# Kernel optimization log

Measured on AMD Instinct MI355X. Metric: run time of the kernel, lower is better.

The kernel has to match this reference:

```python
import jax, jax.numpy as jnp
import numpy as np

NUM_ORI = 8      # num_orientations
P = 7            # pooled height/width (out_size)
S = 2            # num_samples (sampling grid per bin side)
SCALE = 0.25     # spatial_scale
CLOCKWISE = False


def setup_inputs() -> dict:
    key = jax.random.key(0)
    kf, kb, kc, ks, ka = jax.random.split(key, 5)
    B, C, H, W = 2, 256, 256, 256   # C = 32 channel groups x 8 orientations
    R = 512
    features = jax.random.normal(kf, (B, C, H, W), dtype=jnp.float32)
    img = H / SCALE                 # image-space extent (1024)
    batch_idx = jax.random.randint(kb, (R,), 0, B).astype(jnp.float32)
    ctr = jax.random.uniform(kc, (R, 2), minval=0.0, maxval=img)
    wh = jax.random.uniform(ks, (R, 2), minval=32.0, maxval=img * 0.25)
    ang = jax.random.uniform(ka, (R,), minval=-np.pi, maxval=np.pi)
    rois = jnp.concatenate([batch_idx[:, None], ctr, wh, ang[:, None]], axis=1)
    return {"features": features, "rois": rois}


def _riroi_align_rotated(features, rois):
    B, C, H, W = features.shape
    O = NUM_ORI
    Cg = C // O
    R = rois.shape[0]
    f32 = features.dtype

    b = rois[:, 0].astype(jnp.int32)
    cx = rois[:, 1] * SCALE
    cy = rois[:, 2] * SCALE
    rw = jnp.maximum(rois[:, 3] * SCALE, 1.0)
    rh = jnp.maximum(rois[:, 4] * SCALE, 1.0)
    theta = rois[:, 5]

    # --- orientation channel alignment (uses original-sign theta) ---
    ind_f = theta * O / (2.0 * np.pi)
    ind_floor = jnp.floor(ind_f)
    l_var = ind_f - ind_floor                         # (R,)
    r_var = 1.0 - l_var
    ind = jnp.mod(ind_floor.astype(jnp.int32), O)     # start channel, (R,)
    o = jnp.arange(O)
    ind_rot = jnp.mod(o[None, :] - ind[:, None], O)   # (R,O)
    ind_rot_p = jnp.mod(ind_rot + 1, O)

    if CLOCKWISE:
        theta = -theta

    # --- rotated sampling grid, (R, Ph, Pw, Sy, Sx) ---
    bin_h = rh / P
    bin_w = rw / P
    pidx = jnp.arange(P, dtype=f32)
    sidx = jnp.arange(S, dtype=f32)
    yy = (-rh[:, None, None] / 2.0 + pidx[None, :, None] * bin_h[:, None, None]
          + (sidx[None, None, :] + 0.5) * bin_h[:, None, None] / S)   # (R,Ph,Sy)
    xx = (-rw[:, None, None] / 2.0 + pidx[None, :, None] * bin_w[:, None, None]
          + (sidx[None, None, :] + 0.5) * bin_w[:, None, None] / S)   # (R,Pw,Sx)
    ct = jnp.cos(theta)[:, None, None, None, None]
    st = jnp.sin(theta)[:, None, None, None, None]
    X = xx[:, None, :, None, :]   # (R,1,Pw,1,Sx)
    Y = yy[:, :, None, :, None]   # (R,Ph,1,Sy,1)
    x = (X * ct - Y * st + cx[:, None, None, None, None]).reshape(R, -1)  # (R,K)
    y = (X * st + Y * ct + cy[:, None, None, None, None]).reshape(R, -1)

    # --- bilinear interpolation (matches mmcv bilinear_interpolate) ---
    valid = ~((y < -1.0) | (y > H) | (x < -1.0) | (x > W))
    yc = jnp.clip(y, 0.0, None)
    xc = jnp.clip(x, 0.0, None)
    y0 = yc.astype(jnp.int32)
    x0 = xc.astype(jnp.int32)
    hi_y = y0 >= H - 1
    hi_x = x0 >= W - 1
    y1 = jnp.where(hi_y, H - 1, y0 + 1)
    y0 = jnp.where(hi_y, H - 1, y0)
    yc = jnp.where(hi_y, y0.astype(f32), yc)
    x1 = jnp.where(hi_x, W - 1, x0 + 1)
    x0 = jnp.where(hi_x, W - 1, x0)
    xc = jnp.where(hi_x, x0.astype(f32), xc)
    ly = yc - y0.astype(f32); hy = 1.0 - ly
    lx = xc - x0.astype(f32); hx = 1.0 - lx
    vf = valid.astype(f32)
    w1 = (hy * hx * vf)[..., None]
    w2 = (hy * lx * vf)[..., None]
    w3 = (ly * hx * vf)[..., None]
    w4 = (ly * lx * vf)[..., None]

    bb = b[:, None]                                     # (R,1) -> broadcast (R,K)
    v = (w1 * features[bb, :, y0, x0] + w2 * features[bb, :, y0, x1]
         + w3 * features[bb, :, y1, x0] + w4 * features[bb, :, y1, x1])  # (R,K,C)

    # average over the SxS sample grid per bin
    v = v.reshape(R, P, P, S, S, Cg, O).mean(axis=(3, 4))   # (R,P,P,Cg,O)

    # orientation channel cyclic blend
    idx = ind_rot[:, None, None, None, :]               # (R,1,1,1,O)
    idx_p = ind_rot_p[:, None, None, None, :]
    rb = r_var[:, None, None, None, None]
    lb = l_var[:, None, None, None, None]
    out = rb * jnp.take_along_axis(v, idx, axis=4) + lb * jnp.take_along_axis(v, idx_p, axis=4)
    # (R,Ph,Pw,Cg,O) -> (R, Cg, O, Ph, Pw) -> (R, C, Ph, Pw)
    return out.transpose(0, 3, 4, 1, 2).reshape(R, Cg * O, P, P)


def reference(features, rois):
    return _riroi_align_rotated(features, rois)
```

## Files before the change

kernel.cpp:

```cpp
#include <hip/hip_runtime.h>


#define NORI 8
#define PBIN 7
#define NPIX 49
#define CCH 256
#define HH 256
#define WW 256
#define PTOT (HH * WW)

__global__ __launch_bounds__(256) void nchw_to_nhwc_kernel(
    const float* __restrict__ feat, float* __restrict__ nhwc)
{
    __shared__ float tile[128 * 68];
    const int t = threadIdx.x;
    int blk = blockIdx.x;
    const int b  = blk >> 11;
    blk &= 2047;
    const int p0 = (blk >> 2) * 128;
    const int c0 = (blk & 3) * 64;

    const int pl    = t & 127;
    const int chalf = (t >> 7) * 4;

    const float* __restrict__ src = feat + ((size_t)b * CCH + c0) * PTOT + p0 + pl;

    #pragma unroll
    for (int k = 0; k < 8; ++k) {
        const int cl = chalf + 8 * k;
        float4 v;
        v.x = src[(size_t)(cl + 0) * PTOT];
        v.y = src[(size_t)(cl + 1) * PTOT];
        v.z = src[(size_t)(cl + 2) * PTOT];
        v.w = src[(size_t)(cl + 3) * PTOT];
        *reinterpret_cast<float4*>(&tile[pl * 68 + cl]) = v;
    }
    __syncthreads();

    float* __restrict__ dst = nhwc + ((size_t)b * PTOT + p0) * CCH + c0;
    #pragma unroll
    for (int k = 0; k < 8; ++k) {
        const int flat = t + 256 * k;
        const int p    = flat >> 4;
        const int c4   = (flat & 15) * 4;
        const float4 w = *reinterpret_cast<const float4*>(&tile[p * 68 + c4]);
        *reinterpret_cast<float4*>(dst + (size_t)p * CCH + c4) = w;
    }
}

__global__ __launch_bounds__(256) void riroi_gather_nhwc_kernel(
    const float* __restrict__ nhwc,
    const float* __restrict__ rois,
    float* __restrict__ out)
{
    __shared__ float stage[64 * NPIX];

    const int r   = blockIdx.x >> 2;
    const int q   = blockIdx.x & 3;
    const int t   = threadIdx.x;
    const int cl4 = (t & 15) * 4;
    const int c4  = q * 64 + cl4;
    const int pixlane = t >> 4;

    const float* roi = rois + r * 6;
    const int   b     = (int)roi[0];
    const float cx    = roi[1] * 0.25f;
    const float cy    = roi[2] * 0.25f;
    const float rw    = fmaxf(roi[3] * 0.25f, 1.0f);
    const float rh    = fmaxf(roi[4] * 0.25f, 1.0f);
    const float theta = roi[5];

    const float ind_f     = theta * (8.0f / 6.283185307179586f);
    const float ind_floor = floorf(ind_f);
    const float l_var     = ind_f - ind_floor;
    const float r_var     = 1.0f - l_var;
    const int   ind       = (((int)ind_floor % NORI) + NORI) % NORI;

    const float bin_h = rh * (1.0f / (float)PBIN);
    const float bin_w = rw * (1.0f / (float)PBIN);
    const float ct = cosf(theta);
    const float st = sinf(theta);
    const float Hf = (float)HH, Wf = (float)WW;

    const float* __restrict__ fb = nhwc + (size_t)b * PTOT * CCH;

    #pragma unroll
    for (int k = 0; k < 4; ++k) {
        const int pix = pixlane + 16 * k;
        if (pix < NPIX) {
            const int ph = pix / PBIN;
            const int pw = pix - ph * PBIN;
            const float y_base = -rh * 0.5f + (float)ph * bin_h;
            const float x_base = -rw * 0.5f + (float)pw * bin_w;

            float ax = 0.0f, ay = 0.0f, az = 0.0f, aw = 0.0f;
            #pragma unroll
            for (int sy = 0; sy < 2; ++sy) {
                #pragma unroll
                for (int sx = 0; sx < 2; ++sx) {
                    const float Y = y_base + ((float)sy + 0.5f) * bin_h * 0.5f;
                    const float X = x_base + ((float)sx + 0.5f) * bin_w * 0.5f;
                    const float x = X * ct - Y * st + cx;
                    const float y = X * st + Y * ct + cy;

                    const bool valid = !((y < -1.0f) || (y > Hf) || (x < -1.0f) || (x > Wf));
                    float yc = fmaxf(y, 0.0f);
                    float xc = fmaxf(x, 0.0f);
                    int y0 = (int)yc;
                    int x0 = (int)xc;
                    int y1, x1;
                    if (y0 >= HH - 1) { y0 = HH - 1; y1 = HH - 1; yc = (float)y0; }
                    else              { y1 = y0 + 1; }
                    if (x0 >= WW - 1) { x0 = WW - 1; x1 = WW - 1; xc = (float)x0; }
                    else              { x1 = x0 + 1; }

                    const float ly = yc - (float)y0, hy = 1.0f - ly;
                    const float lx = xc - (float)x0, hx = 1.0f - lx;
                    const float vf = valid ? 1.0f : 0.0f;
                    const float w1 = hy * hx * vf;
                    const float w2 = hy * lx * vf;
                    const float w3 = ly * hx * vf;
                    const float w4 = ly * lx * vf;

                    const float4 f00 = *reinterpret_cast<const float4*>(
                        fb + ((size_t)(y0 * WW + x0)) * CCH + c4);
                    const float4 f01 = *reinterpret_cast<const float4*>(
                        fb + ((size_t)(y0 * WW + x1)) * CCH + c4);
                    const float4 f10 = *reinterpret_cast<const float4*>(
                        fb + ((size_t)(y1 * WW + x0)) * CCH + c4);
                    const float4 f11 = *reinterpret_cast<const float4*>(
                        fb + ((size_t)(y1 * WW + x1)) * CCH + c4);

                    ax += w1 * f00.x + w2 * f01.x + w3 * f10.x + w4 * f11.x;
                    ay += w1 * f00.y + w2 * f01.y + w3 * f10.y + w4 * f11.y;
                    az += w1 * f00.z + w2 * f01.z + w3 * f10.z + w4 * f11.z;
                    aw += w1 * f00.w + w2 * f01.w + w3 * f10.w + w4 * f11.w;
                }
            }
            stage[(cl4 + 0) * NPIX + pix] = ax * 0.25f;
            stage[(cl4 + 1) * NPIX + pix] = ay * 0.25f;
            stage[(cl4 + 2) * NPIX + pix] = az * 0.25f;
            stage[(cl4 + 3) * NPIX + pix] = aw * 0.25f;
        }
    }
    __syncthreads();

    float* __restrict__ dst = out + (size_t)r * (CCH * NPIX) + q * (64 * NPIX);
    #pragma unroll
    for (int k = 0; k < 13; ++k) {
        const int i = t + 256 * k;
        if (i < 64 * NPIX) {
            const int c   = i / NPIX;
            const int pix = i - c * NPIX;
            const int o   = c & (NORI - 1);
            const int s0  = (c & ~(NORI - 1)) | ((o - ind + 8) & (NORI - 1));
            const int s1  = (c & ~(NORI - 1)) | ((o - ind + 9) & (NORI - 1));
            dst[i] = r_var * stage[s0 * NPIX + pix] + l_var * stage[s1 * NPIX + pix];
        }
    }
}

__global__ __launch_bounds__(256) void riroi_align_rotated_kernel(
    const float* __restrict__ feat, const float* __restrict__ rois,
    float* __restrict__ out, int C, int H, int W)
{
    const int blk = blockIdx.x;
    const int r   = blk / (PBIN * PBIN);
    const int pix = blk % (PBIN * PBIN);
    const int ph  = pix / PBIN;
    const int pw  = pix % PBIN;
    const int c   = threadIdx.x;
    const int o   = c & (NORI - 1);

    const float* roi = rois + r * 6;
    const int   b     = (int)roi[0];
    const float cx    = roi[1] * 0.25f;
    const float cy    = roi[2] * 0.25f;
    const float rw    = fmaxf(roi[3] * 0.25f, 1.0f);
    const float rh    = fmaxf(roi[4] * 0.25f, 1.0f);
    const float theta = roi[5];

    const float ind_f     = theta * (8.0f / 6.283185307179586f);
    const float ind_floor = floorf(ind_f);
    const float l_var     = ind_f - ind_floor;
    const float r_var     = 1.0f - l_var;
    const int ind = (((int)ind_floor % NORI) + NORI) % NORI;

    const float bin_h = rh * (1.0f / (float)PBIN);
    const float bin_w = rw * (1.0f / (float)PBIN);
    const float ct = cosf(theta);
    const float st = sinf(theta);

    const float* __restrict__ fbc = feat + ((size_t)b * C + c) * (size_t)(H * W);
    const float Hf = (float)H, Wf = (float)W;
    const float y_base = -rh * 0.5f + (float)ph * bin_h;
    const float x_base = -rw * 0.5f + (float)pw * bin_w;

    float acc = 0.0f;
    #pragma unroll
    for (int sy = 0; sy < 2; ++sy) {
        #pragma unroll
        for (int sx = 0; sx < 2; ++sx) {
            const float Y = y_base + ((float)sy + 0.5f) * bin_h * 0.5f;
            const float X = x_base + ((float)sx + 0.5f) * bin_w * 0.5f;
            float x = X * ct - Y * st + cx;
            float y = X * st + Y * ct + cy;
            const bool valid = !((y < -1.0f) || (y > Hf) || (x < -1.0f) || (x > Wf));
            float yc = fmaxf(y, 0.0f);
            float xc = fmaxf(x, 0.0f);
            int y0 = (int)yc;
            int x0 = (int)xc;
            int y1, x1;
            if (y0 >= H - 1) { y0 = H - 1; y1 = H - 1; yc = (float)y0; }
            else             { y1 = y0 + 1; }
            if (x0 >= W - 1) { x0 = W - 1; x1 = W - 1; xc = (float)x0; }
            else             { x1 = x0 + 1; }
            const float ly = yc - (float)y0, hy = 1.0f - ly;
            const float lx = xc - (float)x0, hx = 1.0f - lx;
            const float vf = valid ? 1.0f : 0.0f;
            const float w1 = hy * hx * vf, w2 = hy * lx * vf;
            const float w3 = ly * hx * vf, w4 = ly * lx * vf;
            acc += w1 * fbc[y0 * W + x0] + w2 * fbc[y0 * W + x1]
                 + w3 * fbc[y1 * W + x0] + w4 * fbc[y1 * W + x1];
        }
    }
    const float v = acc * 0.25f;
    const int lane  = threadIdx.x & 63;
    const int base  = lane & ~(NORI - 1);
    const int osrc  = (o - ind + NORI) & (NORI - 1);
    const float v0 = __shfl(v, base | osrc, 64);
    const float v1 = __shfl(v, base | ((osrc + 1) & (NORI - 1)), 64);
    out[((size_t)r * C + c) * (PBIN * PBIN) + ph * PBIN + pw] = r_var * v0 + l_var * v1;
}

extern "C" void kernel_launch(void* const* d_in, const int* in_sizes, int n_in,
                              void* d_out, int out_size, void* d_ws, size_t ws_size,
                              hipStream_t stream) {
    const float* feat = (const float*)d_in[0];
    const float* rois = (const float*)d_in[1];
    float* out = (float*)d_out;

    const int R = in_sizes[1] / 6;
    const int B = in_sizes[0] / (CCH * PTOT);
    const size_t need = (size_t)B * PTOT * CCH * sizeof(float);

    if (ws_size >= need) {
        float* nhwc = (float*)d_ws;
        nchw_to_nhwc_kernel<<<dim3(B * 2048), dim3(256), 0, stream>>>(feat, nhwc);
        riroi_gather_nhwc_kernel<<<dim3(R * 4), dim3(256), 0, stream>>>(nhwc, rois, out);
    } else {
        riroi_align_rotated_kernel<<<dim3(R * PBIN * PBIN), dim3(256), 0, stream>>>(
            feat, rois, out, CCH, HH, WW);
    }
}
```

Measured before the change: 267.9 us.

## Rewrite NCHW-to-NHWC transpose with float4 loads, shuffle 4x4 transpose, swizzled LDS

The layout transpose kernel now loads float4 vectors along the pixel dimension instead of scalar strided loads. It transposes 4x4 sub-blocks in registers with cross-lane shuffles and writes them into a 128x128 shared tile, using an XOR swizzle instead of padding to avoid bank conflicts. Tiles grow to 128 channels, which halves the grid. This targets load efficiency of the memory-bound transpose, at the cost of higher register and LDS use (64KB per block) and therefore lower occupancy.

```diff
diff --git a/kernel.cpp b/kernel.cpp
--- a/kernel.cpp
+++ b/kernel.cpp
@@ -12,39 +12,67 @@
 __global__ __launch_bounds__(256) void nchw_to_nhwc_kernel(
     const float* __restrict__ feat, float* __restrict__ nhwc)
 {
-    __shared__ float tile[128 * 68];
+    __shared__ float tile[128 * 128];
+
     const int t = threadIdx.x;
-    int blk = blockIdx.x;
-    const int b  = blk >> 11;
-    blk &= 2047;
-    const int p0 = (blk >> 2) * 128;
-    const int c0 = (blk & 3) * 64;
-
-    const int pl    = t & 127;
-    const int chalf = (t >> 7) * 4;
-
-    const float* __restrict__ src = feat + ((size_t)b * CCH + c0) * PTOT + p0 + pl;
-
+    const int l = t & 63;
+    const int w = t >> 6;
+    const int blk = blockIdx.x;
+    const int b  = blk >> 10;
+    const int rest = blk & 1023;
+    const int p0 = (rest >> 1) << 7;
+    const int c0 = (rest & 1) << 7;
+
+    const int cb = c0 + 32 * w;
+
+    float4 v[16];
     #pragma unroll
     for (int k = 0; k < 8; ++k) {
-        const int cl = chalf + 8 * k;
-        float4 v;
-        v.x = src[(size_t)(cl + 0) * PTOT];
-        v.y = src[(size_t)(cl + 1) * PTOT];
-        v.z = src[(size_t)(cl + 2) * PTOT];
-        v.w = src[(size_t)(cl + 3) * PTOT];
-        *reinterpret_cast<float4*>(&tile[pl * 68 + cl]) = v;
+        #pragma unroll
+        for (int h = 0; h < 2; ++h) {
+            const int c  = cb + 4 * k + (l & 3);
+            const int p  = p0 + 64 * h + 4 * (l >> 2);
+            v[k * 2 + h] = *reinterpret_cast<const float4*>(
+                feat + ((size_t)b * CCH + c) * PTOT + p);
+        }
+    }
+
+    #pragma unroll
+    for (int k = 0; k < 8; ++k) {
+        #pragma unroll
+        for (int h = 0; h < 2; ++h) {
+            float4 a = v[k * 2 + h];
+            {
+                const float e0 = (l & 1) ? a.x : a.y;
+                const float e1 = (l & 1) ? a.z : a.w;
+                const float r0 = __shfl_xor(e0, 1, 64);
+                const float r1 = __shfl_xor(e1, 1, 64);
+                if (l & 1) { a.x = r0; a.z = r1; } else { a.y = r0; a.w = r1; }
+            }
+            {
+                const float f0 = (l & 2) ? a.x : a.z;
+                const float f1 = (l & 2) ? a.y : a.w;
+                const float s0 = __shfl_xor(f0, 2, 64);
+                const float s1 = __shfl_xor(f1, 2, 64);
+                if (l & 2) { a.x = s0; a.y = s1; } else { a.z = s0; a.w = s1; }
+            }
+            const int p_local = 64 * h + l;
+            const int cq = 8 * w + k;
+            const int cqs = cq ^ (p_local & 7);
+            *reinterpret_cast<float4*>(&tile[p_local * 128 + cqs * 4]) = a;
+        }
     }
     __syncthreads();
 
     float* __restrict__ dst = nhwc + ((size_t)b * PTOT + p0) * CCH + c0;
     #pragma unroll
-    for (int k = 0; k < 8; ++k) {
-        const int flat = t + 256 * k;
-        const int p    = flat >> 4;
-        const int c4   = (flat & 15) * 4;
-        const float4 w = *reinterpret_cast<const float4*>(&tile[p * 68 + c4]);
-        *reinterpret_cast<float4*>(dst + (size_t)p * CCH + c4) = w;
+    for (int j = 0; j < 16; ++j) {
+        const int flat = t + 256 * j;
+        const int p    = flat >> 5;
+        const int cq   = flat & 31;
+        const int cqs  = cq ^ (p & 7);
+        const float4 a = *reinterpret_cast<const float4*>(&tile[p * 128 + cqs * 4]);
+        *reinterpret_cast<float4*>(dst + (size_t)p * CCH + cq * 4) = a;
     }
 }
 
@@ -246,7 +274,7 @@
 
     if (ws_size >= need) {
         float* nhwc = (float*)d_ws;
-        nchw_to_nhwc_kernel<<<dim3(B * 2048), dim3(256), 0, stream>>>(feat, nhwc);
+        nchw_to_nhwc_kernel<<<dim3(B * 1024), dim3(256), 0, stream>>>(feat, nhwc);
         riroi_gather_nhwc_kernel<<<dim3(R * 4), dim3(256), 0, stream>>>(nhwc, rois, out);
     } else {
         riroi_align_rotated_kernel<<<dim3(R * PBIN * PBIN), dim3(256), 0, stream>>>(
```

After: 266.6 us. Within noise of the previous version (-0.5%).
